# Optimization experiments

Measured on AMD Instinct MI355X. Metric: run time of the kernel, lower is better.

The kernel has to match this reference:

```python
import jax, jax.numpy as jnp
import numpy as np

V, D, H, F, L, B, T = 32000, 512, 8, 2048, 4, 4, 1024
DK = D // H
S = 0.02  # init scale


def setup_inputs() -> dict:
    key = jax.random.key(0)
    ks = jax.random.split(key, 10)
    inp = {
        'x': jax.random.randint(ks[0], (B, T), 0, V),
        'embed': jax.random.normal(ks[1], (V, D), jnp.float32) * S,
        'Wq': jax.random.normal(ks[2], (L, D, D), jnp.float32) * S,
        'bq': jnp.zeros((L, D), jnp.float32),
        'Wk': jax.random.normal(ks[3], (L, D, D), jnp.float32) * S,
        'bk': jnp.zeros((L, D), jnp.float32),
        'Wv': jax.random.normal(ks[4], (L, D, D), jnp.float32) * S,
        'bv': jnp.zeros((L, D), jnp.float32),
        'Wo': jax.random.normal(ks[5], (L, D, D), jnp.float32) * S,
        'bo': jnp.zeros((L, D), jnp.float32),
        'ln1_s': jnp.ones((L, D), jnp.float32),
        'ln1_b': jnp.zeros((L, D), jnp.float32),
        'W1': jax.random.normal(ks[6], (L, D, F), jnp.float32) * S,
        'b1': jnp.zeros((L, F), jnp.float32),
        'W2': jax.random.normal(ks[7], (L, F, D), jnp.float32) * S,
        'b2': jnp.zeros((L, D), jnp.float32),
        'ln2_s': jnp.ones((L, D), jnp.float32),
        'ln2_b': jnp.zeros((L, D), jnp.float32),
        'lnf_s': jnp.ones((D,), jnp.float32),
        'lnf_b': jnp.zeros((D,), jnp.float32),
        'Wl': jax.random.normal(ks[8], (D, V), jnp.float32) * S,
        'bl': jnp.zeros((V,), jnp.float32),
    }
    return inp


def _layernorm(x, s, b, eps=1e-5):
    m = jnp.mean(x, axis=-1, keepdims=True)
    v = jnp.mean(jnp.square(x - m), axis=-1, keepdims=True)
    return (x - m) * jax.lax.rsqrt(v + eps) * s + b


def _forward(x, embed, Wq, bq, Wk, bk, Wv, bv, Wo, bo, ln1_s, ln1_b,
             W1, b1, W2, b2, ln2_s, ln2_b, lnf_s, lnf_b, Wl, bl):
    Bb, Tt = x.shape
    emb = embed.at[0].set(0.0)  # padding_idx = 0
    h = emb[x]  # [B,T,D]
    # sinusoidal positional encoding
    pos = jnp.arange(Tt, dtype=jnp.float32)[:, None]
    div = jnp.exp(jnp.arange(0, D, 2, dtype=jnp.float32) * (-np.log(10000.0) / D))
    pe = jnp.zeros((Tt, D), jnp.float32)
    pe = pe.at[:, 0::2].set(jnp.sin(pos * div)).at[:, 1::2].set(jnp.cos(pos * div))
    h = h + pe[None]
    # additive causal mask: 0 on/below diag, -inf above
    causal = jnp.triu(jnp.full((Tt, Tt), -jnp.inf, jnp.float32), 1)
    scale = 1.0 / np.sqrt(DK)
    for l in range(L):
        q = (h @ Wq[l] + bq[l]).reshape(Bb, Tt, H, DK)
        k = (h @ Wk[l] + bk[l]).reshape(Bb, Tt, H, DK)
        v = (h @ Wv[l] + bv[l]).reshape(Bb, Tt, H, DK)
        scores = jnp.einsum('bqhd,bkhd->bhqk', q, k) * scale + causal
        attn = jax.nn.softmax(scores, axis=-1)  # dropout=0 -> identity
        o = jnp.einsum('bhqk,bkhd->bqhd', attn, v).reshape(Bb, Tt, D)
        o = o @ Wo[l] + bo[l]
        h = _layernorm(h + o, ln1_s[l], ln1_b[l])
        ff = jax.nn.gelu(h @ W1[l] + b1[l], approximate=False) @ W2[l] + b2[l]
        h = _layernorm(h + ff, ln2_s[l], ln2_b[l])
    h = _layernorm(h, lnf_s, lnf_b)
    return h @ Wl + bl  # [B,T,V] logits


def reference(x, embed, Wq, bq, Wk, bk, Wv, bv, Wo, bo, ln1_s, ln1_b,
              W1, b1, W2, b2, ln2_s, ln2_b, lnf_s, lnf_b, Wl, bl):
    return _forward(x, embed, Wq, bq, Wk, bk, Wv, bv, Wo, bo, ln1_s, ln1_b,
                    W1, b1, W2, b2, ln2_s, ln2_b, lnf_s, lnf_b, Wl, bl)
```

## Files before the change

### kernel.cpp

```cpp
#include <hip/hip_runtime.h>
#include <math.h>

#define Mtot 4096
#define Dd   512
#define Hh   8
#define DKk  64
#define TT   1024
#define Ff   2048
#define Ll   4
#define Vv   32000

typedef __attribute__((ext_vector_type(8))) short bf16x8;
typedef __attribute__((ext_vector_type(4))) float f32x4;
typedef unsigned short u16;

__device__ __forceinline__ u16 f2b(float f) {
    union { float f; unsigned u; } x; x.f = f;
    unsigned r = x.u + 0x7fffu + ((x.u >> 16) & 1u);
    return (u16)(r >> 16);
}

typedef const __attribute__((address_space(1))) unsigned int* gp_t;
typedef __attribute__((address_space(3))) unsigned int* lp_t;
#define GLOAD_LDS16(g, l) __builtin_amdgcn_global_load_lds((gp_t)(const void*)(g), (lp_t)(void*)(l), 16, 0, 0)
#define SBAR  __builtin_amdgcn_s_barrier()
#define SCHED0 __builtin_amdgcn_sched_barrier(0)

#define SWZ(row, c)  ((c) ^ (((row) & 7) << 3))

__global__ __launch_bounds__(256) void embed_pe_kernel(const int* __restrict__ x,
                                                       const float* __restrict__ embed,
                                                       float* __restrict__ h,
                                                       u16* __restrict__ hb) {
    int idx = blockIdx.x * 256 + threadIdx.x;
    int d  = idx & (Dd - 1);
    int bt = idx >> 9;
    int t  = bt & (TT - 1);
    int tok = x[bt];
    float val = (tok == 0) ? 0.0f : embed[(size_t)tok * Dd + d];
    int de = d & ~1;
    float ang = (float)t * expf((float)de * (-9.210340371976184f / (float)Dd));
    val += (d & 1) ? cosf(ang) : sinf(ang);
    h[idx] = val;
    hb[idx] = f2b(val);
}

__global__ __launch_bounds__(256) void transpose_all(const float* __restrict__ Wq, const float* __restrict__ Wk,
                                                     const float* __restrict__ Wv, const float* __restrict__ Wo,
                                                     const float* __restrict__ W1, const float* __restrict__ W2,
                                                     const float* __restrict__ Wl,
                                                     u16* __restrict__ WqkvT, u16* __restrict__ WoT,
                                                     u16* __restrict__ W1T, u16* __restrict__ W2T,
                                                     u16* __restrict__ WlT) {
    __shared__ float t[32][33];
    int id = blockIdx.x;
    const float* src; u16* dst; int K, N, tx, ty;
    if (id < 12288) {
        int l = id / 3072, r = id - l * 3072;
        if (r < 768) {
            int which = r >> 8, t2 = r & 255;
            src = (which == 0 ? Wq : which == 1 ? Wk : Wv) + (size_t)l * 262144;
            dst = WqkvT + (size_t)l * 786432 + (size_t)which * 262144;
            K = 512; N = 512; ty = t2 >> 4; tx = t2 & 15;
        } else if (r < 1024) {
            int t2 = r - 768;
            src = Wo + (size_t)l * 262144; dst = WoT + (size_t)l * 262144;
            K = 512; N = 512; ty = t2 >> 4; tx = t2 & 15;
        } else if (r < 2048) {
            int t2 = r - 1024;
            src = W1 + (size_t)l * 1048576; dst = W1T + (size_t)l * 1048576;
            K = 512; N = 2048; ty = t2 >> 6; tx = t2 & 63;
        } else {
            int t2 = r - 2048;
            src = W2 + (size_t)l * 1048576; dst = W2T + (size_t)l * 1048576;
            K = 2048; N = 512; ty = t2 >> 4; tx = t2 & 15;
        }
    } else {
        int t2 = id - 12288;
        src = Wl; dst = WlT; K = 512; N = 32000;
        ty = t2 / 1000; tx = t2 - ty * 1000;
    }
    int n0 = tx * 32, k0 = ty * 32;
    int tid = threadIdx.x, c = tid & 31, rr = tid >> 5;
    #pragma unroll
    for (int i = 0; i < 4; i++)
        t[rr + i * 8][c] = src[(size_t)(k0 + rr + i * 8) * N + n0 + c];
    __syncthreads();
    #pragma unroll
    for (int i = 0; i < 4; i++)
        dst[(size_t)(n0 + rr + i * 8) * K + k0 + c] = f2b(t[c][rr + i * 8]);
}

__global__ __launch_bounds__(256) void biaspack_kernel(const float* __restrict__ bq,
                                                       const float* __restrict__ bk,
                                                       const float* __restrict__ bv,
                                                       float* __restrict__ bqkv) {
    int idx = blockIdx.x * 256 + threadIdx.x;
    int l = idx / 1536, j = idx - l * 1536;
    float v = (j < 512) ? bq[l * 512 + j] : (j < 1024) ? bk[l * 512 + j - 512] : bv[l * 512 + j - 1024];
    bqkv[idx] = v;
}

template<int ACT, int OUTB, int QKVMODE>
__global__ __launch_bounds__(256, 2) void mfma_gemm(const u16* __restrict__ A,
                                                    const u16* __restrict__ BT,
                                                    const float* __restrict__ bias,
                                                    float* __restrict__ outF,
                                                    u16* __restrict__ outB,
                                                    u16* __restrict__ vtb,
                                                    int M, int N, int K, int gx) {
    __shared__ __align__(16) u16 As[2][128 * 64];
    __shared__ __align__(16) u16 Bs[2][128 * 64];
    int tid = threadIdx.x;
    int lane = tid & 63, w = tid >> 6;
    int nwg = gridDim.x, flat = blockIdx.x;
    int wg = (flat & 7) * (nwg >> 3) + (flat >> 3);
    int bm = wg / gx, bn = wg - bm * gx;
    int wr = w >> 1, wc = w & 1;
    int fr = lane & 15, fq = lane >> 4;

    int sr = lane >> 3, sc = lane & 7;
    int scol = (sc ^ sr) * 8;
    const u16* Ab = A  + (size_t)(bm * 128 + w * 32 + sr) * K + scol;
    const u16* Bb = BT + (size_t)(bn * 128 + w * 32 + sr) * K + scol;
    u16* lA = &As[0][0] + w * 2048;
    u16* lB = &Bs[0][0] + w * 2048;

    f32x4 acc[4][4] = {};
    int nk = K >> 6;

#define STAGE(buf, kt)                                                     \
    {   int ko = (kt) * 64;                                                \
        GLOAD_LDS16(Ab + ko,          lA + (buf) * (128 * 64));            \
        GLOAD_LDS16(Ab + 8 * K + ko,  lA + (buf) * (128 * 64) + 512);      \
        GLOAD_LDS16(Ab + 16 * K + ko, lA + (buf) * (128 * 64) + 1024);     \
        GLOAD_LDS16(Ab + 24 * K + ko, lA + (buf) * (128 * 64) + 1536);     \
        GLOAD_LDS16(Bb + ko,          lB + (buf) * (128 * 64));            \
        GLOAD_LDS16(Bb + 8 * K + ko,  lB + (buf) * (128 * 64) + 512);      \
        GLOAD_LDS16(Bb + 16 * K + ko, lB + (buf) * (128 * 64) + 1024);     \
        GLOAD_LDS16(Bb + 24 * K + ko, lB + (buf) * (128 * 64) + 1536); }

    STAGE(0, 0);
    STAGE(1, 1);

    int cur = 0;
    for (int kt = 0; kt < nk; kt++) {
        if (kt + 1 < nk) { asm volatile("s_waitcnt vmcnt(8)" ::: "memory"); }
        else             { asm volatile("s_waitcnt vmcnt(0)" ::: "memory"); }
        SBAR;
        SCHED0;
        bf16x8 a[4][2], b[4][2];
        #pragma unroll
        for (int m = 0; m < 4; m++) {
            int row = wr * 64 + m * 16 + fr;
            a[m][0] = *(const bf16x8*)&As[cur][row * 64 + ((fq ^ (row & 7)) * 8)];
            a[m][1] = *(const bf16x8*)&As[cur][row * 64 + (((fq + 4) ^ (row & 7)) * 8)];
        }
        #pragma unroll
        for (int n = 0; n < 4; n++) {
            int row = wc * 64 + n * 16 + fr;
            b[n][0] = *(const bf16x8*)&Bs[cur][row * 64 + ((fq ^ (row & 7)) * 8)];
            b[n][1] = *(const bf16x8*)&Bs[cur][row * 64 + (((fq + 4) ^ (row & 7)) * 8)];
        }
        __builtin_amdgcn_s_setprio(1);
        #pragma unroll
        for (int m = 0; m < 4; m++)
            #pragma unroll
            for (int n = 0; n < 4; n++) {
                acc[m][n] = __builtin_amdgcn_mfma_f32_16x16x32_bf16(a[m][0], b[n][0], acc[m][n], 0, 0, 0);
                acc[m][n] = __builtin_amdgcn_mfma_f32_16x16x32_bf16(a[m][1], b[n][1], acc[m][n], 0, 0, 0);
            }
        __builtin_amdgcn_s_setprio(0);
        SCHED0;
        SBAR;
        SCHED0;
        if (kt + 2 < nk) STAGE(cur, kt + 2);
        cur ^= 1;
    }
#undef STAGE

    #pragma unroll
    for (int m = 0; m < 4; m++) {
        #pragma unroll
        for (int n = 0; n < 4; n++) {
            int col = bn * 128 + wc * 64 + n * 16 + fr;
            float bs = bias ? bias[col] : 0.0f;
            if (QKVMODE && bn >= 8) {
                int hh = (col - 1024) >> 6, d = (col - 1024) & 63;
                #pragma unroll
                for (int r = 0; r < 4; r++) {
                    int row = bm * 128 + wr * 64 + m * 16 + fq * 4 + r;
                    int bb = row >> 10, t = row & 1023;
                    vtb[(((size_t)bb * Hh + hh) * 64 + d) * 1024 + t] = f2b(acc[m][n][r] + bs);
                }
            } else {
                #pragma unroll
                for (int r = 0; r < 4; r++) {
                    int row = bm * 128 + wr * 64 + m * 16 + fq * 4 + r;
                    float v = acc[m][n][r] + bs;
                    if (ACT == 1) v = 0.5f * v * (1.0f + erff(v * 0.7071067811865475f));
                    if (OUTB) outB[(size_t)row * N + col] = f2b(v);
                    else      outF[(size_t)row * N + col] = v;
                }
            }
        }
    }
}

__global__ __launch_bounds__(256) void attn_mfma(const u16* __restrict__ qkv,
                                                 const u16* __restrict__ vtb,
                                                 u16* __restrict__ ob) {
    int qt = (int)gridDim.x - 1 - (int)blockIdx.x;
    int hh = blockIdx.y, b = blockIdx.z;
    __shared__ __align__(16) u16 Qs[64 * 64];
    __shared__ __align__(16) u16 Ks[64 * 64];
    __shared__ __align__(16) u16 Vs[64 * 64];
    __shared__ __align__(16) u16 Ps[4][16 * 64];
    int tid = threadIdx.x;
    int lane = tid & 63, w = tid >> 6;
    int fr = lane & 15, fq = lane >> 4;
    int q0 = qt * 64;
    int sr = tid >> 2, sc0 = (tid & 3) * 16;

    bf16x8 rk0, rk1, rv0, rv1;
    bf16x8 sk0, sk1, sv0, sv1;

    auto load_a = [&](int kt) {
        const u16* srcK = qkv + ((size_t)(b * TT + kt * 64 + sr)) * 1536 + 512 + hh * 64 + sc0;
        rk0 = *(const bf16x8*)srcK; rk1 = *(const bf16x8*)(srcK + 8);
        const u16* srcV = vtb + (((size_t)(b * Hh + hh)) * 64 + sr) * 1024 + kt * 64 + sc0;
        rv0 = *(const bf16x8*)srcV; rv1 = *(const bf16x8*)(srcV + 8);
    };
    auto load_b = [&](int kt) {
        const u16* srcK = qkv + ((size_t)(b * TT + kt * 64 + sr)) * 1536 + 512 + hh * 64 + sc0;
        sk0 = *(const bf16x8*)srcK; sk1 = *(const bf16x8*)(srcK + 8);
        const u16* srcV = vtb + (((size_t)(b * Hh + hh)) * 64 + sr) * 1024 + kt * 64 + sc0;
        sv0 = *(const bf16x8*)srcV; sv1 = *(const bf16x8*)(srcV + 8);
    };
    auto store_a = [&]() {
        *(bf16x8*)&Ks[sr * 64 + SWZ(sr, sc0)]     = rk0;
        *(bf16x8*)&Ks[sr * 64 + SWZ(sr, sc0 + 8)] = rk1;
        *(bf16x8*)&Vs[sr * 64 + SWZ(sr, sc0)]     = rv0;
        *(bf16x8*)&Vs[sr * 64 + SWZ(sr, sc0 + 8)] = rv1;
    };
    auto store_b = [&]() {
        *(bf16x8*)&Ks[sr * 64 + SWZ(sr, sc0)]     = sk0;
        *(bf16x8*)&Ks[sr * 64 + SWZ(sr, sc0 + 8)] = sk1;
        *(bf16x8*)&Vs[sr * 64 + SWZ(sr, sc0)]     = sv0;
        *(bf16x8*)&Vs[sr * 64 + SWZ(sr, sc0 + 8)] = sv1;
    };

    load_a(0);
    {
        const u16* src = qkv + ((size_t)(b * TT + q0 + sr)) * 1536 + hh * 64 + sc0;
        bf16x8 v0 = *(const bf16x8*)src;
        bf16x8 v1 = *(const bf16x8*)(src + 8);
        *(bf16x8*)&Qs[sr * 64 + SWZ(sr, sc0)]     = v0;
        *(bf16x8*)&Qs[sr * 64 + SWZ(sr, sc0 + 8)] = v1;
    }
    __syncthreads();
    bf16x8 aq0 = *(const bf16x8*)&Qs[(w * 16 + fr) * 64 + SWZ(w * 16 + fr, fq * 8)];
    bf16x8 aq1 = *(const bf16x8*)&Qs[(w * 16 + fr) * 64 + SWZ(w * 16 + fr, 32 + fq * 8)];

    f32x4 oa[4] = {};
    float mreg[4], lreg[4];
    #pragma unroll
    for (int i = 0; i < 4; i++) { mreg[i] = -1e30f; lreg[i] = 0.0f; }

    auto compute_tile = [&](int kt) {
        f32x4 sa[4] = {};
        __builtin_amdgcn_s_setprio(1);
        #pragma unroll
        for (int nt = 0; nt < 4; nt++) {
            int krow = nt * 16 + fr;
            bf16x8 b0 = *(const bf16x8*)&Ks[krow * 64 + SWZ(krow, fq * 8)];
            bf16x8 b1 = *(const bf16x8*)&Ks[krow * 64 + SWZ(krow, 32 + fq * 8)];
            sa[nt] = __builtin_amdgcn_mfma_f32_16x16x32_bf16(aq0, b0, sa[nt], 0, 0, 0);
            sa[nt] = __builtin_amdgcn_mfma_f32_16x16x32_bf16(aq1, b1, sa[nt], 0, 0, 0);
        }
        __builtin_amdgcn_s_setprio(0);

        float p[4][4];
        int qg = w * 16 + fq * 4;
        bool diag = (kt == qt);
        #pragma unroll
        for (int nt = 0; nt < 4; nt++)
            #pragma unroll
            for (int i = 0; i < 4; i++) {
                float s = sa[nt][i] * 0.125f;
                if (diag && (nt * 16 + fr > qg + i)) s = -1e30f;
                p[nt][i] = s;
            }

        float mnew[4], fscale[4];
        #pragma unroll
        for (int i = 0; i < 4; i++) {
            float v = fmaxf(fmaxf(p[0][i], p[1][i]), fmaxf(p[2][i], p[3][i]));
            v = fmaxf(v, __shfl_xor(v, 1));
            v = fmaxf(v, __shfl_xor(v, 2));
            v = fmaxf(v, __shfl_xor(v, 4));
            v = fmaxf(v, __shfl_xor(v, 8));
            mnew[i] = fmaxf(mreg[i], v);
            fscale[i] = __expf(mreg[i] - mnew[i]);
            mreg[i] = mnew[i];
        }
        #pragma unroll
        for (int i = 0; i < 4; i++) {
            float sum = 0.f;
            #pragma unroll
            for (int nt = 0; nt < 4; nt++) {
                float e = __expf(p[nt][i] - mnew[i]);
                p[nt][i] = e;
                sum += e;
            }
            sum += __shfl_xor(sum, 1);
            sum += __shfl_xor(sum, 2);
            sum += __shfl_xor(sum, 4);
            sum += __shfl_xor(sum, 8);
            lreg[i] = lreg[i] * fscale[i] + sum;
        }
        #pragma unroll
        for (int nn = 0; nn < 4; nn++)
            #pragma unroll
            for (int i = 0; i < 4; i++)
                oa[nn][i] *= fscale[i];

        u16* ps = &Ps[w][0];
        #pragma unroll
        for (int nt = 0; nt < 4; nt++)
            #pragma unroll
            for (int i = 0; i < 4; i++) {
                int row = fq * 4 + i, col = nt * 16 + fr;
                ps[row * 64 + SWZ(row, col)] = f2b(p[nt][i]);
            }
        bf16x8 pa0 = *(const bf16x8*)&ps[fr * 64 + SWZ(fr, fq * 8)];
        bf16x8 pa1 = *(const bf16x8*)&ps[fr * 64 + SWZ(fr, 32 + fq * 8)];
        __builtin_amdgcn_s_setprio(1);
        #pragma unroll
        for (int nn = 0; nn < 4; nn++) {
            int drow = nn * 16 + fr;
            bf16x8 vb0 = *(const bf16x8*)&Vs[drow * 64 + SWZ(drow, fq * 8)];
            bf16x8 vb1 = *(const bf16x8*)&Vs[drow * 64 + SWZ(drow, 32 + fq * 8)];
            oa[nn] = __builtin_amdgcn_mfma_f32_16x16x32_bf16(pa0, vb0, oa[nn], 0, 0, 0);
            oa[nn] = __builtin_amdgcn_mfma_f32_16x16x32_bf16(pa1, vb1, oa[nn], 0, 0, 0);
        }
        __builtin_amdgcn_s_setprio(0);
    };

    int kt = 0;
    for (;;) {
        SCHED0; SBAR;
        store_a();
        if (kt + 1 <= qt) load_b(kt + 1);
        asm volatile("s_waitcnt lgkmcnt(0)" ::: "memory");
        SBAR; SCHED0;
        compute_tile(kt);
        if (++kt > qt) break;

        SCHED0; SBAR;
        store_b();
        if (kt + 1 <= qt) load_a(kt + 1);
        asm volatile("s_waitcnt lgkmcnt(0)" ::: "memory");
        SBAR; SCHED0;
        compute_tile(kt);
        if (++kt > qt) break;
    }

    #pragma unroll
    for (int i = 0; i < 4; i++) {
        float inv = 1.0f / lreg[i];
        size_t row = (size_t)(b * TT + q0 + w * 16 + fq * 4 + i) * Dd + hh * 64;
        #pragma unroll
        for (int nn = 0; nn < 4; nn++)
            ob[row + nn * 16 + fr] = f2b(oa[nn][i] * inv);
    }
}

__global__ __launch_bounds__(256) void ln_kernel(float* __restrict__ h,
                                                 const float* __restrict__ d1,
                                                 const float* __restrict__ gs,
                                                 const float* __restrict__ gb,
                                                 u16* __restrict__ hb) {
    int w = threadIdx.x >> 6, lane = threadIdx.x & 63;
    int row = (blockIdx.x << 2) + w;
    size_t base = (size_t)row * Dd + lane * 8;
    f32x4 v0 = *(const f32x4*)&h[base];
    f32x4 v1 = *(const f32x4*)&h[base + 4];
    if (d1) { v0 += *(const f32x4*)&d1[base]; v1 += *(const f32x4*)&d1[base + 4]; }
    float s = v0[0] + v0[1] + v0[2] + v0[3] + v1[0] + v1[1] + v1[2] + v1[3];
    #pragma unroll
    for (int st = 1; st < 64; st <<= 1) s += __shfl_xor(s, st);
    float m = s * (1.0f / Dd);
    float q = 0.f;
    #pragma unroll
    for (int j = 0; j < 4; j++) { float a = v0[j] - m, b = v1[j] - m; q += a * a + b * b; }
    #pragma unroll
    for (int st = 1; st < 64; st <<= 1) q += __shfl_xor(q, st);
    float r = rsqrtf(q * (1.0f / Dd) + 1e-5f);
    f32x4 g0 = *(const f32x4*)&gs[lane * 8],     g1 = *(const f32x4*)&gs[lane * 8 + 4];
    f32x4 c0 = *(const f32x4*)&gb[lane * 8],     c1 = *(const f32x4*)&gb[lane * 8 + 4];
    f32x4 y0, y1;
    bf16x8 yb;
    #pragma unroll
    for (int j = 0; j < 4; j++) {
        y0[j] = (v0[j] - m) * r * g0[j] + c0[j];
        y1[j] = (v1[j] - m) * r * g1[j] + c1[j];
        yb[j]     = (short)f2b(y0[j]);
        yb[j + 4] = (short)f2b(y1[j]);
    }
    *(f32x4*)&h[base]     = y0;
    *(f32x4*)&h[base + 4] = y1;
    *(bf16x8*)&hb[base]   = yb;
}

extern "C" void kernel_launch(void* const* d_in, const int* in_sizes, int n_in,
                              void* d_out, int out_size, void* d_ws, size_t ws_size,
                              hipStream_t stream) {
    const int*   x     = (const int*)  d_in[0];
    const float* embed = (const float*)d_in[1];
    const float* Wq    = (const float*)d_in[2];
    const float* bq    = (const float*)d_in[3];
    const float* Wk    = (const float*)d_in[4];
    const float* bk    = (const float*)d_in[5];
    const float* Wv    = (const float*)d_in[6];
    const float* bv    = (const float*)d_in[7];
    const float* Wo    = (const float*)d_in[8];
    const float* bo    = (const float*)d_in[9];
    const float* ln1_s = (const float*)d_in[10];
    const float* ln1_b = (const float*)d_in[11];
    const float* W1    = (const float*)d_in[12];
    const float* b1    = (const float*)d_in[13];
    const float* W2    = (const float*)d_in[14];
    const float* b2    = (const float*)d_in[15];
    const float* ln2_s = (const float*)d_in[16];
    const float* ln2_b = (const float*)d_in[17];
    const float* lnf_s = (const float*)d_in[18];
    const float* lnf_b = (const float*)d_in[19];
    const float* Wl    = (const float*)d_in[20];
    const float* bl    = (const float*)d_in[21];

    char* wp = (char*)d_ws;
    float* h    = (float*)wp;  wp += (size_t)Mtot * Dd * 4;
    float* pb   = (float*)wp;  wp += (size_t)Mtot * Dd * 4;
    u16*   hb   = (u16*)wp;    wp += (size_t)Mtot * Dd * 2;
    u16*   qkvb = (u16*)wp;    wp += (size_t)Mtot * 1536 * 2;
    u16*   vtb  = (u16*)wp;    wp += (size_t)Mtot * Dd * 2;
    u16*   obb  = (u16*)wp;    wp += (size_t)Mtot * Dd * 2;
    u16*   fbb  = (u16*)wp;    wp += (size_t)Mtot * Ff * 2;
    u16*   WlT  = (u16*)wp;    wp += (size_t)Vv * Dd * 2;
    float* bqkv = (float*)wp;  wp += (size_t)Ll * 1536 * 4;

    char* op = (char*)d_out;
    u16* WqkvT = (u16*)op;  op += (size_t)Ll * 1536 * Dd * 2;
    u16* WoT   = (u16*)op;  op += (size_t)Ll * Dd * Dd * 2;
    u16* W1T   = (u16*)op;  op += (size_t)Ll * Ff * Dd * 2;
    u16* W2T   = (u16*)op;  op += (size_t)Ll * Dd * Ff * 2;

    transpose_all<<<28288, 256, 0, stream>>>(Wq, Wk, Wv, Wo, W1, W2, Wl, WqkvT, WoT, W1T, W2T, WlT);
    biaspack_kernel<<<24, 256, 0, stream>>>(bq, bk, bv, bqkv);
    embed_pe_kernel<<<(Mtot * Dd) / 256, 256, 0, stream>>>(x, embed, h, hb);

    for (int l = 0; l < Ll; l++) {
        mfma_gemm<0, 1, 1><<<(1536 / 128) * (Mtot / 128), 256, 0, stream>>>(
            hb, WqkvT + (size_t)l * 1536 * Dd, bqkv + l * 1536, nullptr, qkvb, vtb,
            Mtot, 1536, Dd, 1536 / 128);
        attn_mfma<<<dim3(TT / 64, Hh, 4), 256, 0, stream>>>(qkvb, vtb, obb);
        mfma_gemm<0, 0, 0><<<(Dd / 128) * (Mtot / 128), 256, 0, stream>>>(
            obb, WoT + (size_t)l * Dd * Dd, bo + l * Dd, pb, nullptr, nullptr,
            Mtot, Dd, Dd, Dd / 128);
        ln_kernel<<<Mtot / 4, 256, 0, stream>>>(h, pb, ln1_s + l * Dd, ln1_b + l * Dd, hb);
        mfma_gemm<1, 1, 0><<<(Ff / 128) * (Mtot / 128), 256, 0, stream>>>(
            hb, W1T + (size_t)l * Ff * Dd, b1 + l * Ff, nullptr, fbb, nullptr,
            Mtot, Ff, Dd, Ff / 128);
        mfma_gemm<0, 0, 0><<<(Dd / 128) * (Mtot / 128), 256, 0, stream>>>(
            fbb, W2T + (size_t)l * Dd * Ff, b2 + l * Dd, pb, nullptr, nullptr,
            Mtot, Dd, Ff, Dd / 128);
        ln_kernel<<<Mtot / 4, 256, 0, stream>>>(h, pb, ln2_s + l * Dd, ln2_b + l * Dd, hb);
    }

    ln_kernel<<<Mtot / 4, 256, 0, stream>>>(h, nullptr, lnf_s, lnf_b, hb);
    mfma_gemm<0, 0, 0><<<(Vv / 128) * (Mtot / 128), 256, 0, stream>>>(
        hb, WlT, bl, (float*)d_out, nullptr, nullptr, Mtot, Vv, Dd, Vv / 128);
}
```

Baseline: 828.5 us.

## Use 256x256-tile GEMM kernel with 512 threads for vocab projection

New measurement: 821.1 us. About the same (-0.9%).

```diff
diff --git a/kernel.cpp b/kernel.cpp
--- a/kernel.cpp
+++ b/kernel.cpp
@@ -207,6 +207,92 @@
     }
 }
 
+__global__ __launch_bounds__(512, 1) void mfma_gemm256(const u16* __restrict__ A,
+                                                       const u16* __restrict__ BT,
+                                                       const float* __restrict__ bias,
+                                                       float* __restrict__ outF,
+                                                       int M, int N, int K, int gy) {
+    __shared__ __align__(16) u16 As[2][256 * 64];
+    __shared__ __align__(16) u16 Bs[2][256 * 64];
+    int tid = threadIdx.x;
+    int lane = tid & 63, w = tid >> 6;
+    int nwg = gridDim.x, flat = blockIdx.x;
+    int wg = (flat & 7) * (nwg >> 3) + (flat >> 3);
+    int bm = wg & (gy - 1), bn = wg >> 4;
+    int wr = w >> 2, wc = w & 3;
+    int fr = lane & 15, fq = lane >> 4;
+
+    int sr8 = lane >> 3, sc = lane & 7;
+    int scol = (sc ^ sr8) * 8;
+    const u16* Ab = A  + (size_t)(bm * 256 + w * 32 + sr8) * K + scol;
+    const u16* Bb = BT + (size_t)(bn * 256 + w * 32 + sr8) * K + scol;
+
+    f32x4 acc[8][4] = {};
+    int nk = K >> 6;
+
+#define STAGE256(buf, kt)                                                    \
+    {   int ko = (kt) * 64;                                                  \
+        GLOAD_LDS16(Ab + ko,          &As[buf][(w * 32 +  0) * 64]);         \
+        GLOAD_LDS16(Ab + 8 * K + ko,  &As[buf][(w * 32 +  8) * 64]);         \
+        GLOAD_LDS16(Ab + 16 * K + ko, &As[buf][(w * 32 + 16) * 64]);         \
+        GLOAD_LDS16(Ab + 24 * K + ko, &As[buf][(w * 32 + 24) * 64]);         \
+        GLOAD_LDS16(Bb + ko,          &Bs[buf][(w * 32 +  0) * 64]);         \
+        GLOAD_LDS16(Bb + 8 * K + ko,  &Bs[buf][(w * 32 +  8) * 64]);         \
+        GLOAD_LDS16(Bb + 16 * K + ko, &Bs[buf][(w * 32 + 16) * 64]);         \
+        GLOAD_LDS16(Bb + 24 * K + ko, &Bs[buf][(w * 32 + 24) * 64]); }
+
+    STAGE256(0, 0);
+    STAGE256(1, 1);
+
+    int cur = 0;
+    for (int kt = 0; kt < nk; kt++) {
+        if (kt + 1 < nk) { asm volatile("s_waitcnt vmcnt(8)" ::: "memory"); }
+        else             { asm volatile("s_waitcnt vmcnt(0)" ::: "memory"); }
+        SBAR;
+        SCHED0;
+        bf16x8 b[4][2];
+        #pragma unroll
+        for (int n = 0; n < 4; n++) {
+            int row = wc * 64 + n * 16 + fr;
+            b[n][0] = *(const bf16x8*)&Bs[cur][row * 64 + ((fq ^ (row & 7)) * 8)];
+            b[n][1] = *(const bf16x8*)&Bs[cur][row * 64 + (((fq + 4) ^ (row & 7)) * 8)];
+        }
+        #pragma unroll
+        for (int m = 0; m < 8; m++) {
+            int row = wr * 128 + m * 16 + fr;
+            bf16x8 a0 = *(const bf16x8*)&As[cur][row * 64 + ((fq ^ (row & 7)) * 8)];
+            bf16x8 a1 = *(const bf16x8*)&As[cur][row * 64 + (((fq + 4) ^ (row & 7)) * 8)];
+            __builtin_amdgcn_s_setprio(1);
+            #pragma unroll
+            for (int n = 0; n < 4; n++) {
+                acc[m][n] = __builtin_amdgcn_mfma_f32_16x16x32_bf16(a0, b[n][0], acc[m][n], 0, 0, 0);
+                acc[m][n] = __builtin_amdgcn_mfma_f32_16x16x32_bf16(a1, b[n][1], acc[m][n], 0, 0, 0);
+            }
+            __builtin_amdgcn_s_setprio(0);
+        }
+        SCHED0;
+        SBAR;
+        SCHED0;
+        if (kt + 2 < nk) STAGE256(cur, kt + 2);
+        cur ^= 1;
+    }
+#undef STAGE256
+
+    #pragma unroll
+    for (int m = 0; m < 8; m++) {
+        #pragma unroll
+        for (int n = 0; n < 4; n++) {
+            int col = bn * 256 + wc * 64 + n * 16 + fr;
+            float bs = bias[col];
+            #pragma unroll
+            for (int r = 0; r < 4; r++) {
+                int row = bm * 256 + wr * 128 + m * 16 + fq * 4 + r;
+                outF[(size_t)row * N + col] = acc[m][n][r] + bs;
+            }
+        }
+    }
+}
+
 __global__ __launch_bounds__(256) void attn_mfma(const u16* __restrict__ qkv,
                                                  const u16* __restrict__ vtb,
                                                  u16* __restrict__ ob) {
@@ -479,6 +565,6 @@
     }
 
     ln_kernel<<<Mtot / 4, 256, 0, stream>>>(h, nullptr, lnf_s, lnf_b, hb);
-    mfma_gemm<0, 0, 0><<<(Vv / 128) * (Mtot / 128), 256, 0, stream>>>(
-        hb, WlT, bl, (float*)d_out, nullptr, nullptr, Mtot, Vv, Dd, Vv / 128);
-}
+    mfma_gemm256<<<(Vv / 256) * (Mtot / 256), 512, 0, stream>>>(
+        hb, WlT, bl, (float*)d_out, Mtot, Vv, Dd, Mtot / 256);
+}
```
